# Optimization experiments

Measured on AMD Instinct MI355X. Metric: run time of the kernel, lower is better.

Reference implementation:

```python
import jax, jax.numpy as jnp
import numpy as np

BS, SL, N_AGENTS, OBS_DIM, STATE_DIM, N_EDGES, HID = 32, 512, 32, 96, 1024, 64, 256


def _hgcn(w_line, x, H):
    # x: [B, n, 1]; H: [B, n, E]. Faithful to torch HGCN:
    # A = D^{-1/2} H |W| B^{-1} H^T D^{-1/2}, with D, B built from detached H/|W|,
    # inf entries (from 0^{-1} / 0^{-0.5}) zeroed. Diagonal matmuls are implicit scalings.
    w_abs = jnp.abs(w_line)
    Hd = jax.lax.stop_gradient(H)
    d = jnp.einsum('bne,e->bn', Hd, jax.lax.stop_gradient(w_abs))  # [B, n]
    d_is = jnp.where(d > 0, jax.lax.rsqrt(jnp.where(d > 0, d, 1.0)), 0.0)
    b = jnp.sum(Hd, axis=-2)  # [B, E]
    b_inv = jnp.where(b > 0, 1.0 / jnp.where(b > 0, b, 1.0), 0.0)
    t = d_is[..., None] * x                       # D^{-1/2} x
    s = jnp.einsum('bne,bnk->bek', H, t)          # H^T (...)
    s = s * (w_abs[None, :] * b_inv)[..., None]   # |W| B^{-1} (diagonals commute)
    y = jnp.einsum('bne,bek->bnk', H, s)          # H (...)
    return d_is[..., None] * y                    # D^{-1/2} (...)


def _mlp(x, w1, b1, w2, b2):
    return jax.nn.relu(x @ w1 + b1) @ w2 + b2


def setup_inputs() -> dict:
    key = jax.random.key(0)
    ks = jax.random.split(key, 24)
    f = jax.random.normal
    inp = {
        'agent_qs': f(ks[0], (BS, SL, N_AGENTS), jnp.float32),
        'states': f(ks[1], (BS, SL, STATE_DIM), jnp.float32),
        'indiv_us': f(ks[2], (BS, SL, N_AGENTS, OBS_DIM), jnp.float32),
        'edge_W': f(ks[3], (OBS_DIM, N_EDGES), jnp.float32) * 0.1,
        'edge_b': f(ks[4], (N_EDGES,), jnp.float32) * 0.1,
        'wline1': 1.0 + 0.1 * f(ks[5], (N_EDGES,), jnp.float32),
        'wline2': 1.0 + 0.1 * f(ks[6], (N_EDGES,), jnp.float32),
    }
    names = ['hw1', 'hc1', 'hw', 'hc']
    outs = [N_AGENTS, N_AGENTS, N_AGENTS, 1]
    for i, (nm, od) in enumerate(zip(names, outs)):
        inp[nm + '_w1'] = f(ks[7 + 4 * i], (STATE_DIM, HID), jnp.float32) * 0.05
        inp[nm + '_b1'] = f(ks[8 + 4 * i], (HID,), jnp.float32) * 0.05
        inp[nm + '_w2'] = f(ks[9 + 4 * i], (HID, od), jnp.float32) * 0.05
        inp[nm + '_b2'] = f(ks[10 + 4 * i], (od,), jnp.float32) * 0.05
    return inp


def reference(agent_qs, states, indiv_us, edge_W, edge_b, wline1, wline2,
              hw1_w1, hw1_b1, hw1_w2, hw1_b2, hc1_w1, hc1_b1, hc1_w2, hc1_b2,
              hw_w1, hw_b1, hw_w2, hw_b2, hc_w1, hc_b1, hc_w2, hc_b2):
    bs, sl, n = agent_qs.shape
    q = agent_qs.reshape(-1, n)                               # [B, n]
    u = indiv_us.reshape(-1, n, indiv_us.shape[-1])           # [B, n, obs]
    s = states.reshape(-1, states.shape[-1])                  # [B, state_dim]
    H = jax.nn.relu(u @ edge_W + edge_b)                      # hyper_edge_net -> [B, n, E]
    x = q[..., None]                                          # node_features [B, n, 1]
    qs_tot = _hgcn(wline2, _hgcn(wline1, x, H), H)[..., 0]    # two stacked HGCN encoders
    w1 = jnp.abs(_mlp(s, hw1_w1, hw1_b1, hw1_w2, hw1_b2))
    c1 = _mlp(s, hc1_w1, hc1_b1, hc1_w2, hc1_b2)
    qt = jax.nn.elu(qs_tot * w1 + c1)
    w = jnp.abs(_mlp(s, hw_w1, hw_b1, hw_w2, hw_b2))
    c = _mlp(s, hc_w1, hc_b1, hc_w2, hc_b2)[..., 0]
    q_tot = jnp.sum(qt * w, axis=-1) + c
    return q_tot.reshape(bs, sl, 1)
```

## Files before the change

kernel.cpp:

```cpp
#include <hip/hip_runtime.h>
#include <cstdint>

typedef _Float16 f16;
typedef _Float16 f16x2 __attribute__((ext_vector_type(2)));
typedef _Float16 f16x4 __attribute__((ext_vector_type(4)));
typedef _Float16 f16x8 __attribute__((ext_vector_type(8)));
typedef float f32x4 __attribute__((ext_vector_type(4)));

#define AS1U const __attribute__((address_space(1))) unsigned int
#define AS3U __attribute__((address_space(3))) unsigned int

__device__ __forceinline__ void gload_lds16(const void* g, void* l) {
    __builtin_amdgcn_global_load_lds((AS1U*)g, (AS3U*)l, 16, 0, 0);
}

#define WSYNC() asm volatile("s_waitcnt lgkmcnt(0)" ::: "memory")

#define BATCH 16384
#define NAG   32
#define OBS   96
#define SDIM  1024
#define NE    64
#define HIDN  256
#define NH    1024

#define NB_ST 1024
#define NB_PW 256
#define NB_SM 101
#define NB_FRONT (NB_ST + NB_PW + NB_SM)

__global__ __launch_bounds__(256) void k_front(
    const float* __restrict__ states,
    const float* __restrict__ w1a, const float* __restrict__ w1b,
    const float* __restrict__ w1c, const float* __restrict__ w1d,
    const float* __restrict__ b1a, const float* __restrict__ b1b,
    const float* __restrict__ b1c, const float* __restrict__ b1d,
    const float* __restrict__ w2a, const float* __restrict__ w2b,
    const float* __restrict__ w2c, const float* __restrict__ w2d,
    f16* __restrict__ states16, f16* __restrict__ W1t, float* __restrict__ b1cat,
    f16* __restrict__ W2t, f16* __restrict__ hcw2) {
    __shared__ float tile[64 * 65];
    const int tid = threadIdx.x;
    int bid = blockIdx.x;

    if (bid < NB_ST) {
        int i = bid * 256 + tid;
        const int n4 = BATCH * SDIM / 4;
        const int stride = NB_ST * 256;
        for (; i < n4; i += stride) {
            float4 v = ((const float4*)states)[i];
            f16x4 h = { (f16)v.x, (f16)v.y, (f16)v.z, (f16)v.w };
            ((f16x4*)states16)[i] = h;
        }
        return;
    }
    bid -= NB_ST;
    if (bid < NB_PW) {
        int mlp = bid >> 6, rem = bid & 63, kt = rem >> 2, ct = rem & 3;
        const float* src = (mlp == 0) ? w1a : (mlp == 1) ? w1b : (mlp == 2) ? w1c : w1d;
        int k0 = kt * 64, c0 = ct * 64;
        for (int i = tid; i < 4096; i += 256) {
            int kk = i >> 6, cc = i & 63;
            tile[kk * 65 + cc] = src[(size_t)(k0 + kk) * 256 + c0 + cc];
        }
        __syncthreads();
        for (int i = tid; i < 4096; i += 256) {
            int cc = i >> 6, kk = i & 63;
            W1t[(size_t)(mlp * 256 + c0 + cc) * 1024 + k0 + kk] = (f16)tile[kk * 65 + cc];
        }
        return;
    }
    bid -= NB_PW;
    {
        int i = bid * 256 + tid;
        if (i < 24576) {
            int mp = i >> 13, rem = i & 8191, oo = rem >> 8, kk = rem & 255;
            const float* src = (mp == 0) ? w2a : (mp == 1) ? w2b : w2c;
            W2t[i] = (f16)src[kk * 32 + oo];
        } else if (i < 24832) {
            int k = i - 24576;
            hcw2[k] = (f16)w2d[k];
        } else if (i < 25856) {
            int n = i - 24832;
            int mlp = n >> 8, c = n & 255;
            const float* bsrc = (mlp == 0) ? b1a : (mlp == 1) ? b1b : (mlp == 2) ? b1c : b1d;
            b1cat[n] = bsrc[c];
        }
    }
}

__global__ __launch_bounds__(256) void k_gemm1(
    const f16* __restrict__ A, const f16* __restrict__ B,
    const float* __restrict__ b1cat, const f16* __restrict__ W2t,
    const f16* __restrict__ hcw2, float* __restrict__ Pp) {
    __shared__ __align__(16) char smem[33792];
    f16* As = (f16*)smem;
    f16* Bs = (f16*)(smem + 16384);
    f16* Ts = (f16*)smem;

    const int tid = threadIdx.x;
    const int w = tid >> 6, l = tid & 63;
    const int p = blockIdx.x;
    const int xcd = p & 7, slot = p >> 3;
    const int region = slot >> 6, rs = slot & 63;
    const int mt = (xcd * 2 + region) * 8 + (rs >> 3);
    const int nt = rs & 7;
    const int m0 = mt * 128, n0 = nt * 128;
    const int wm = w >> 1, wn = w & 1;
    const int lm = l & 15, lk = l >> 4;
    const int srow = l >> 3;
    const int scol = (l & 7) * 8;

    f32x4 acc[4][4];
    #pragma unroll
    for (int i = 0; i < 4; i++)
        #pragma unroll
        for (int j = 0; j < 4; j++) acc[i][j] = (f32x4){0.f, 0.f, 0.f, 0.f};

    for (int kt = 0; kt < 16; kt++) {
        #pragma unroll
        for (int i = 0; i < 4; i++) {
            int c = w * 4 + i;
            int row = c * 8 + srow;
            gload_lds16(&A[(size_t)(m0 + row) * 1024 + kt * 64 + scol], &As[c * 512]);
            gload_lds16(&B[(size_t)(n0 + row) * 1024 + kt * 64 + scol], &Bs[c * 512]);
        }
        __syncthreads();
        #pragma unroll
        for (int ks = 0; ks < 2; ks++) {
            f16x8 a[4], bb[4];
            #pragma unroll
            for (int i = 0; i < 4; i++)
                a[i] = *(const f16x8*)&As[(wm * 64 + i * 16 + lm) * 64 + ks * 32 + lk * 8];
            #pragma unroll
            for (int j = 0; j < 4; j++)
                bb[j] = *(const f16x8*)&Bs[(wn * 64 + j * 16 + lm) * 64 + ks * 32 + lk * 8];
            #pragma unroll
            for (int i = 0; i < 4; i++)
                #pragma unroll
                for (int j = 0; j < 4; j++)
                    acc[i][j] = __builtin_amdgcn_mfma_f32_16x16x32_f16(a[i], bb[j], acc[i][j], 0, 0, 0);
        }
        __syncthreads();
    }

    float bj[4];
    #pragma unroll
    for (int j = 0; j < 4; j++) bj[j] = b1cat[n0 + wn * 64 + j * 16 + lm];
    #pragma unroll
    for (int i = 0; i < 4; i++)
        #pragma unroll
        for (int r = 0; r < 4; r++) {
            int row = wm * 64 + i * 16 + lk * 4 + r;
            #pragma unroll
            for (int j = 0; j < 4; j++) {
                int col = wn * 64 + j * 16 + lm;
                float v = acc[i][j][r] + bj[j];
                Ts[row * 132 + col] = (f16)(v > 0.f ? v : 0.f);
            }
        }
    __syncthreads();

    const int mlp = nt >> 1, kh = nt & 1;
    const int rbase = w * 32;
    if (mlp < 3) {
        const f16* wb = W2t + mlp * 8192 + kh * 128;
        f32x4 acc2[2][2];
        acc2[0][0] = (f32x4){0,0,0,0}; acc2[0][1] = (f32x4){0,0,0,0};
        acc2[1][0] = (f32x4){0,0,0,0}; acc2[1][1] = (f32x4){0,0,0,0};
        #pragma unroll
        for (int ks = 0; ks < 4; ks++) {
            f16x8 b0 = *(const f16x8*)&wb[lm * 256 + ks * 32 + lk * 8];
            f16x8 b1 = *(const f16x8*)&wb[(16 + lm) * 256 + ks * 32 + lk * 8];
            #pragma unroll
            for (int i2 = 0; i2 < 2; i2++) {
                f16x8 a = *(const f16x8*)&Ts[(rbase + i2 * 16 + lm) * 132 + ks * 32 + lk * 8];
                acc2[i2][0] = __builtin_amdgcn_mfma_f32_16x16x32_f16(a, b0, acc2[i2][0], 0, 0, 0);
                acc2[i2][1] = __builtin_amdgcn_mfma_f32_16x16x32_f16(a, b1, acc2[i2][1], 0, 0, 0);
            }
        }
        #pragma unroll
        for (int i2 = 0; i2 < 2; i2++)
            #pragma unroll
            for (int j2 = 0; j2 < 2; j2++)
                #pragma unroll
                for (int r = 0; r < 4; r++)
                    Pp[((size_t)kh * BATCH + m0 + rbase + i2 * 16 + lk * 4 + r) * 104
                       + mlp * 32 + j2 * 16 + lm] = acc2[i2][j2][r];
    } else {
        const f16* hc = hcw2 + kh * 128;
        f32x4 acc2[2];
        acc2[0] = (f32x4){0,0,0,0}; acc2[1] = (f32x4){0,0,0,0};
        #pragma unroll
        for (int ks = 0; ks < 4; ks++) {
            f16x8 bz = (f16x8){0,0,0,0,0,0,0,0};
            if (lm == 0) bz = *(const f16x8*)&hc[ks * 32 + lk * 8];
            #pragma unroll
            for (int i2 = 0; i2 < 2; i2++) {
                f16x8 a = *(const f16x8*)&Ts[(rbase + i2 * 16 + lm) * 132 + ks * 32 + lk * 8];
                acc2[i2] = __builtin_amdgcn_mfma_f32_16x16x32_f16(a, bz, acc2[i2], 0, 0, 0);
            }
        }
        if (lm == 0)
            #pragma unroll
            for (int i2 = 0; i2 < 2; i2++)
                #pragma unroll
                for (int r = 0; r < 4; r++)
                    Pp[((size_t)kh * BATCH + m0 + rbase + i2 * 16 + lk * 4 + r) * 104 + 96]
                        = acc2[i2][r];
    }
}

__global__ __launch_bounds__(256, 5) void k_hgcn_ep(
    const float* __restrict__ agent_qs, const float* __restrict__ indiv_us,
    const float* __restrict__ edge_W, const float* __restrict__ edge_b,
    const float* __restrict__ wline1, const float* __restrict__ wline2,
    const float* __restrict__ Pp,
    const float* __restrict__ hw1_b2, const float* __restrict__ hc1_b2,
    const float* __restrict__ hw_b2, const float* __restrict__ hc_b2,
    float* __restrict__ out) {
    __shared__ __align__(16) char arena[32512];
    f16*   eWs   = (f16*)arena;
    float* swa   = (float*)(arena + 13312);
    f16*   HsB   = (f16*)(arena + 13824);
    f16*   svB   = (f16*)(arena + 30720);
    f16*   sttB  = (f16*)(arena + 31232);
    f16*   sdisB = (f16*)(arena + 31488);
    f16*   sbinvB= (f16*)(arena + 32000);

    const int tid = threadIdx.x;
    const int w = tid >> 6, l = tid & 63;
    const int b = blockIdx.x * 4 + w;
    f16* Hw    = HsB + w * (32 * 66);
    f16* sv    = svB + w * 64;
    f16* stt   = sttB + w * 32;
    f16* sdis  = sdisB + w * 64;
    f16* sbinv = sbinvB + w * 64;

    const int nn = l & 31, half = l >> 5;

    float pa0 = 0.f, pa1 = 0.f, pc0 = 0.f, pc1 = 0.f, pw0 = 0.f, pw1 = 0.f;
    float p96a = 0.f, p96b = 0.f, bw1 = 0.f, bc1 = 0.f, bww = 0.f, bhc = 0.f;
    if (half == 0) {
        const float* p0 = Pp + (size_t)b * 104;
        const float* p1 = Pp + (size_t)(BATCH + b) * 104;
        pa0 = p0[nn];      pa1 = p1[nn];
        pc0 = p0[32 + nn]; pc1 = p1[32 + nn];
        pw0 = p0[64 + nn]; pw1 = p1[64 + nn];
        p96a = p0[96];     p96b = p1[96];
        bw1 = hw1_b2[nn];  bc1 = hc1_b2[nn];
        bww = hw_b2[nn];   bhc = hc_b2[0];
    }
    float q = agent_qs[(size_t)b * 32 + nn];

    for (int i = tid; i < 6144; i += 256) {
        int k = i >> 6, n = i & 63;
        eWs[n * 104 + k] = (f16)edge_W[i];
    }
    if (tid < 64) swa[tid] = fabsf(wline1[tid]);
    else if (tid < 128) swa[tid] = fabsf(wline2[tid - 64]);
    __syncthreads();

    const int lm = l & 15, lk = l >> 4;
    const float* ub = indiv_us + (size_t)b * (NAG * OBS);

    #pragma unroll
    for (int mt = 0; mt < 2; mt++) {
        f16x8 af[3];
        #pragma unroll
        for (int ks = 0; ks < 3; ks++) {
            const float* up = ub + (mt * 16 + lm) * 96 + ks * 32 + lk * 8;
            float4 v0 = *(const float4*)up;
            float4 v1 = *(const float4*)(up + 4);
            af[ks] = (f16x8){ (f16)v0.x, (f16)v0.y, (f16)v0.z, (f16)v0.w,
                              (f16)v1.x, (f16)v1.y, (f16)v1.z, (f16)v1.w };
        }
        #pragma unroll
        for (int nt = 0; nt < 4; nt++) {
            f32x4 acc = {0.f, 0.f, 0.f, 0.f};
            #pragma unroll
            for (int ks = 0; ks < 3; ks++) {
                f16x8 bb = *(const f16x8*)&eWs[(nt * 16 + lm) * 104 + ks * 32 + lk * 8];
                acc = __builtin_amdgcn_mfma_f32_16x16x32_f16(af[ks], bb, acc, 0, 0, 0);
            }
            int col = nt * 16 + lm;
            float bias = edge_b[col];
            #pragma unroll
            for (int r = 0; r < 4; r++) {
                int row = mt * 16 + lk * 4 + r;
                float hv = acc[r] + bias;
                Hw[row * 66 + col] = (f16)(hv > 0.f ? hv : 0.f);
            }
        }
    }
    WSYNC();

    float bsum = 0.f;
    #pragma unroll
    for (int n = 0; n < 32; n++) bsum += (float)Hw[n * 66 + l];
    sbinv[l] = (f16)(bsum > 0.f ? 1.f / bsum : 0.f);

    float dd = 0.f;
    #pragma unroll 8
    for (int e2 = 0; e2 < 32; e2++) {
        f16x2 h2 = *(const f16x2*)&Hw[nn * 66 + e2 * 2];
        dd += (float)h2.x * swa[half * 64 + e2 * 2] + (float)h2.y * swa[half * 64 + e2 * 2 + 1];
    }
    float dis = dd > 0.f ? rsqrtf(dd) : 0.f;
    sdis[l] = (f16)dis;
    if (half == 0) stt[nn] = (f16)(dis * q);
    WSYNC();

    float s1 = 0.f;
    #pragma unroll
    for (int n = 0; n < 32; n++) s1 += (float)Hw[n * 66 + l] * (float)stt[n];
    sv[l] = (f16)(s1 * swa[l] * (float)sbinv[l]);
    WSYNC();

    float y1 = 0.f;
    #pragma unroll 8
    for (int e2 = 0; e2 < 32; e2++) {
        f16x2 h2 = *(const f16x2*)&Hw[nn * 66 + e2 * 2];
        f16x2 s2v = *(const f16x2*)&sv[e2 * 2];
        y1 += (float)h2.x * (float)s2v.x + (float)h2.y * (float)s2v.y;
    }
    float x2 = (float)sdis[nn] * y1;
    if (half == 0) stt[nn] = (f16)((float)sdis[32 + nn] * x2);
    WSYNC();

    float s2 = 0.f;
    #pragma unroll
    for (int n = 0; n < 32; n++) s2 += (float)Hw[n * 66 + l] * (float)stt[n];
    sv[l] = (f16)(s2 * swa[64 + l] * (float)sbinv[l]);
    WSYNC();

    float y2 = 0.f;
    #pragma unroll 8
    for (int e2 = 0; e2 < 32; e2++) {
        f16x2 h2 = *(const f16x2*)&Hw[nn * 66 + e2 * 2];
        f16x2 s2v = *(const f16x2*)&sv[e2 * 2];
        y2 += (float)h2.x * (float)s2v.x + (float)h2.y * (float)s2v.y;
    }

    float qsv = (float)sdis[32 + nn] * y2;
    float w1v = fabsf(pa0 + pa1 + bw1);
    float c1v = pc0 + pc1 + bc1;
    float wwv = fabsf(pw0 + pw1 + bww);
    float z = qsv * w1v + c1v;
    float qt = z > 0.f ? z : expm1f(z);
    float val = (half == 0) ? qt * wwv : 0.f;
    val += __shfl_xor(val, 1, 32);
    val += __shfl_xor(val, 2, 32);
    val += __shfl_xor(val, 4, 32);
    val += __shfl_xor(val, 8, 32);
    val += __shfl_xor(val, 16, 32);
    if (l == 0) out[b] = val + p96a + p96b + bhc;
}

extern "C" void kernel_launch(void* const* d_in, const int* in_sizes, int n_in,
                              void* d_out, int out_size, void* d_ws, size_t ws_size,
                              hipStream_t stream) {
    const float* agent_qs = (const float*)d_in[0];
    const float* states   = (const float*)d_in[1];
    const float* indiv_us = (const float*)d_in[2];
    const float* edge_W   = (const float*)d_in[3];
    const float* edge_b   = (const float*)d_in[4];
    const float* wline1   = (const float*)d_in[5];
    const float* wline2   = (const float*)d_in[6];
    const float* hw1_w1 = (const float*)d_in[7];
    const float* hw1_b1 = (const float*)d_in[8];
    const float* hw1_w2 = (const float*)d_in[9];
    const float* hw1_b2 = (const float*)d_in[10];
    const float* hc1_w1 = (const float*)d_in[11];
    const float* hc1_b1 = (const float*)d_in[12];
    const float* hc1_w2 = (const float*)d_in[13];
    const float* hc1_b2 = (const float*)d_in[14];
    const float* hw_w1  = (const float*)d_in[15];
    const float* hw_b1  = (const float*)d_in[16];
    const float* hw_w2  = (const float*)d_in[17];
    const float* hw_b2  = (const float*)d_in[18];
    const float* hc_w1  = (const float*)d_in[19];
    const float* hc_b1  = (const float*)d_in[20];
    const float* hc_w2  = (const float*)d_in[21];
    const float* hc_b2  = (const float*)d_in[22];

    char* ws = (char*)d_ws;
    size_t o_states16 = 0;
    size_t o_W1t  = o_states16 + (size_t)BATCH * SDIM * 2;
    size_t o_b1   = o_W1t + (size_t)NH * SDIM * 2;
    size_t o_W2t  = o_b1 + 4096;
    size_t o_hcw2 = o_W2t + 49152;
    size_t o_Pp   = o_hcw2 + 512;

    f16*   states16 = (f16*)(ws + o_states16);
    f16*   W1t      = (f16*)(ws + o_W1t);
    float* b1cat    = (float*)(ws + o_b1);
    f16*   W2t      = (f16*)(ws + o_W2t);
    f16*   hcw2     = (f16*)(ws + o_hcw2);
    float* Pp       = (float*)(ws + o_Pp);

    k_front<<<NB_FRONT, 256, 0, stream>>>(
        states,
        hw1_w1, hc1_w1, hw_w1, hc_w1, hw1_b1, hc1_b1, hw_b1, hc_b1,
        hw1_w2, hc1_w2, hw_w2, hc_w2,
        states16, W1t, b1cat, W2t, hcw2);
    k_gemm1<<<1024, 256, 0, stream>>>(states16, W1t, b1cat, W2t, hcw2, Pp);
    k_hgcn_ep<<<BATCH / 4, 256, 0, stream>>>(
        agent_qs, indiv_us, edge_W, edge_b, wline1, wline2, Pp,
        hw1_b2, hc1_b2, hw_b2, hc_b2, (float*)d_out);
}
```

Before: 136.5 us.

## Pre-pack GEMM operands in MFMA fragment order and load directly to registers

The front kernel now writes states and W1 in an MFMA-fragment-packed layout, so the GEMM kernel can load operand fragments straight from global memory into registers. This drops the LDS staging and the barriers in the k-loop. The trade-off is that the GEMM k-loop relies on cache and in-flight loads with no LDS reuse, so each wave re-reads shared fragments from L2. The HGCN epilogue also switches its intermediate scratch from fp16 to fp32 and drops the occupancy hint in launch_bounds.

```diff
diff --git a/kernel.cpp b/kernel.cpp
--- a/kernel.cpp
+++ b/kernel.cpp
@@ -6,13 +6,6 @@
 typedef _Float16 f16x4 __attribute__((ext_vector_type(4)));
 typedef _Float16 f16x8 __attribute__((ext_vector_type(8)));
 typedef float f32x4 __attribute__((ext_vector_type(4)));
-
-#define AS1U const __attribute__((address_space(1))) unsigned int
-#define AS3U __attribute__((address_space(3))) unsigned int
-
-__device__ __forceinline__ void gload_lds16(const void* g, void* l) {
-    __builtin_amdgcn_global_load_lds((AS1U*)g, (AS3U*)l, 16, 0, 0);
-}
 
 #define WSYNC() asm volatile("s_waitcnt lgkmcnt(0)" ::: "memory")
 
@@ -24,10 +17,10 @@
 #define HIDN  256
 #define NH    1024
 
-#define NB_ST 1024
-#define NB_PW 256
-#define NB_SM 101
-#define NB_FRONT (NB_ST + NB_PW + NB_SM)
+#define NB_CONV 512
+#define NB_PW   256
+#define NB_SM   101
+#define NB_FRONT (NB_CONV + NB_PW + NB_SM)
 
 __global__ __launch_bounds__(256) void k_front(
     const float* __restrict__ states,
@@ -37,36 +30,60 @@
     const float* __restrict__ b1c, const float* __restrict__ b1d,
     const float* __restrict__ w2a, const float* __restrict__ w2b,
     const float* __restrict__ w2c, const float* __restrict__ w2d,
-    f16* __restrict__ states16, f16* __restrict__ W1t, float* __restrict__ b1cat,
+    f16* __restrict__ App, f16* __restrict__ Bpp, float* __restrict__ b1cat,
     f16* __restrict__ W2t, f16* __restrict__ hcw2) {
-    __shared__ float tile[64 * 65];
+    __shared__ __align__(16) char arena[34816];
     const int tid = threadIdx.x;
+    const int w = tid >> 6, l = tid & 63;
     int bid = blockIdx.x;
 
-    if (bid < NB_ST) {
-        int i = bid * 256 + tid;
-        const int n4 = BATCH * SDIM / 4;
-        const int stride = NB_ST * 256;
-        for (; i < n4; i += stride) {
-            float4 v = ((const float4*)states)[i];
-            f16x4 h = { (f16)v.x, (f16)v.y, (f16)v.z, (f16)v.w };
-            ((f16x4*)states16)[i] = h;
+    if (bid < NB_CONV) {
+        float* tile = (float*)arena;
+        const int mt = bid >> 2, ktg = bid & 3;
+        const int row = tid >> 1, cb = (tid & 1) * 32;
+        for (int kq = 0; kq < 4; kq++) {
+            const int kt = ktg * 4 + kq;
+            const float* src = states + (size_t)(mt * 128 + row) * 1024 + kt * 64 + cb;
+            #pragma unroll
+            for (int q = 0; q < 8; q++)
+                *(float4*)&tile[row * 68 + cb + q * 4] = *(const float4*)(src + q * 4);
+            __syncthreads();
+            f16* dst = App + (size_t)(mt * 16 + kt) * 8192;
+            #pragma unroll
+            for (int cc = 0; cc < 4; cc++) {
+                const int c = w * 4 + cc;
+                const int i8 = c >> 1, ks = c & 1;
+                const float* tr = &tile[(i8 * 16 + (l & 15)) * 68 + ks * 32 + (l >> 4) * 8];
+                float4 u0 = *(const float4*)tr;
+                float4 u1 = *(const float4*)(tr + 4);
+                f16x8 h = { (f16)u0.x, (f16)u0.y, (f16)u0.z, (f16)u0.w,
+                            (f16)u1.x, (f16)u1.y, (f16)u1.z, (f16)u1.w };
+                *(f16x8*)(dst + c * 512 + l * 8) = h;
+            }
+            __syncthreads();
         }
         return;
     }
-    bid -= NB_ST;
+    bid -= NB_CONV;
     if (bid < NB_PW) {
-        int mlp = bid >> 6, rem = bid & 63, kt = rem >> 2, ct = rem & 3;
+        float* tile = (float*)arena;
+        const int mlp = bid >> 6, k64 = (bid >> 2) & 15, c64 = bid & 3;
         const float* src = (mlp == 0) ? w1a : (mlp == 1) ? w1b : (mlp == 2) ? w1c : w1d;
-        int k0 = kt * 64, c0 = ct * 64;
         for (int i = tid; i < 4096; i += 256) {
             int kk = i >> 6, cc = i & 63;
-            tile[kk * 65 + cc] = src[(size_t)(k0 + kk) * 256 + c0 + cc];
+            tile[kk * 65 + cc] = src[(size_t)(k64 * 64 + kk) * 256 + c64 * 64 + cc];
         }
         __syncthreads();
-        for (int i = tid; i < 4096; i += 256) {
-            int cc = i >> 6, kk = i & 63;
-            W1t[(size_t)(mlp * 256 + c0 + cc) * 1024 + k0 + kk] = (f16)tile[kk * 65 + cc];
+        const int nt = mlp * 2 + (c64 >> 1);
+        const int j8 = (c64 & 1) * 4 + w;
+        const int col = w * 16 + (l & 15);
+        #pragma unroll
+        for (int ks = 0; ks < 2; ks++) {
+            const int kk0 = ks * 32 + (l >> 4) * 8;
+            f16x8 h;
+            #pragma unroll
+            for (int e = 0; e < 8; e++) h[e] = (f16)tile[(kk0 + e) * 65 + col];
+            *(f16x8*)(Bpp + ((size_t)((nt * 16 + k64) * 8 + j8) * 2 + ks) * 512 + l * 8) = h;
         }
         return;
     }
@@ -89,27 +106,21 @@
     }
 }
 
-__global__ __launch_bounds__(256) void k_gemm1(
-    const f16* __restrict__ A, const f16* __restrict__ B,
+__global__ __launch_bounds__(256) void k_gemm(
+    const f16* __restrict__ App, const f16* __restrict__ Bpp,
     const float* __restrict__ b1cat, const f16* __restrict__ W2t,
     const f16* __restrict__ hcw2, float* __restrict__ Pp) {
-    __shared__ __align__(16) char smem[33792];
-    f16* As = (f16*)smem;
-    f16* Bs = (f16*)(smem + 16384);
-    f16* Ts = (f16*)smem;
+    __shared__ __align__(16) f16 Ts[128 * 132];
 
     const int tid = threadIdx.x;
     const int w = tid >> 6, l = tid & 63;
+    const int lm = l & 15, lk = l >> 4;
     const int p = blockIdx.x;
     const int xcd = p & 7, slot = p >> 3;
-    const int region = slot >> 6, rs = slot & 63;
-    const int mt = (xcd * 2 + region) * 8 + (rs >> 3);
-    const int nt = rs & 7;
+    const int mt = xcd * 16 + (slot >> 3);
+    const int nt = slot & 7;
     const int m0 = mt * 128, n0 = nt * 128;
     const int wm = w >> 1, wn = w & 1;
-    const int lm = l & 15, lk = l >> 4;
-    const int srow = l >> 3;
-    const int scol = (l & 7) * 8;
 
     f32x4 acc[4][4];
     #pragma unroll
@@ -117,31 +128,28 @@
         #pragma unroll
         for (int j = 0; j < 4; j++) acc[i][j] = (f32x4){0.f, 0.f, 0.f, 0.f};
 
+    const f16* Ab = App + ((size_t)mt * 16 * 16 + wm * 8) * 512 + l * 8;
+    const f16* Bb = Bpp + ((size_t)nt * 16 * 16 + wn * 8) * 512 + l * 8;
+
+    #pragma unroll 4
     for (int kt = 0; kt < 16; kt++) {
-        #pragma unroll
-        for (int i = 0; i < 4; i++) {
-            int c = w * 4 + i;
-            int row = c * 8 + srow;
-            gload_lds16(&A[(size_t)(m0 + row) * 1024 + kt * 64 + scol], &As[c * 512]);
-            gload_lds16(&B[(size_t)(n0 + row) * 1024 + kt * 64 + scol], &Bs[c * 512]);
-        }
-        __syncthreads();
-        #pragma unroll
-        for (int ks = 0; ks < 2; ks++) {
-            f16x8 a[4], bb[4];
-            #pragma unroll
-            for (int i = 0; i < 4; i++)
-                a[i] = *(const f16x8*)&As[(wm * 64 + i * 16 + lm) * 64 + ks * 32 + lk * 8];
-            #pragma unroll
-            for (int j = 0; j < 4; j++)
-                bb[j] = *(const f16x8*)&Bs[(wn * 64 + j * 16 + lm) * 64 + ks * 32 + lk * 8];
+        const f16* Ak = Ab + (size_t)kt * 8192;
+        const f16* Bk = Bb + (size_t)kt * 8192;
+        f16x8 af[4][2], bf[4][2];
+        #pragma unroll
+        for (int i = 0; i < 4; i++)
+            #pragma unroll
+            for (int ks = 0; ks < 2; ks++) {
+                af[i][ks] = *(const f16x8*)(Ak + (i * 2 + ks) * 512);
+                bf[i][ks] = *(const f16x8*)(Bk + (i * 2 + ks) * 512);
+            }
+        #pragma unroll
+        for (int ks = 0; ks < 2; ks++)
             #pragma unroll
             for (int i = 0; i < 4; i++)
                 #pragma unroll
                 for (int j = 0; j < 4; j++)
-                    acc[i][j] = __builtin_amdgcn_mfma_f32_16x16x32_f16(a[i], bb[j], acc[i][j], 0, 0, 0);
-        }
-        __syncthreads();
+                    acc[i][j] = __builtin_amdgcn_mfma_f32_16x16x32_f16(af[i][ks], bf[j][ks], acc[i][j], 0, 0, 0);
     }
 
     float bj[4];
@@ -211,7 +219,7 @@
     }
 }
 
-__global__ __launch_bounds__(256, 5) void k_hgcn_ep(
+__global__ __launch_bounds__(256) void k_hgcn_ep(
     const float* __restrict__ agent_qs, const float* __restrict__ indiv_us,
     const float* __restrict__ edge_W, const float* __restrict__ edge_b,
     const float* __restrict__ wline1, const float* __restrict__ wline2,
@@ -219,23 +227,23 @@
     const float* __restrict__ hw1_b2, const float* __restrict__ hc1_b2,
     const float* __restrict__ hw_b2, const float* __restrict__ hc_b2,
     float* __restrict__ out) {
-    __shared__ __align__(16) char arena[32512];
+    __shared__ __align__(16) char arena[34304];
     f16*   eWs   = (f16*)arena;
     float* swa   = (float*)(arena + 13312);
     f16*   HsB   = (f16*)(arena + 13824);
-    f16*   svB   = (f16*)(arena + 30720);
-    f16*   sttB  = (f16*)(arena + 31232);
-    f16*   sdisB = (f16*)(arena + 31488);
-    f16*   sbinvB= (f16*)(arena + 32000);
+    float* svB   = (float*)(arena + 30720);
+    float* sttB  = (float*)(arena + 31744);
+    float* sdisB = (float*)(arena + 32256);
+    float* sbinvB= (float*)(arena + 33280);
 
     const int tid = threadIdx.x;
     const int w = tid >> 6, l = tid & 63;
     const int b = blockIdx.x * 4 + w;
-    f16* Hw    = HsB + w * (32 * 66);
-    f16* sv    = svB + w * 64;
-    f16* stt   = sttB + w * 32;
-    f16* sdis  = sdisB + w * 64;
-    f16* sbinv = sbinvB + w * 64;
+    f16*   Hw    = HsB + w * (32 * 66);
+    float* sv    = svB + w * 64;
+    float* stt   = sttB + w * 32;
+    float* sdis  = sdisB + w * 64;
+    float* sbinv = sbinvB + w * 64;
 
     const int nn = l & 31, half = l >> 5;
 
@@ -298,7 +306,7 @@
     float bsum = 0.f;
     #pragma unroll
     for (int n = 0; n < 32; n++) bsum += (float)Hw[n * 66 + l];
-    sbinv[l] = (f16)(bsum > 0.f ? 1.f / bsum : 0.f);
+    sbinv[l] = bsum > 0.f ? 1.f / bsum : 0.f;
 
     float dd = 0.f;
     #pragma unroll 8
@@ -307,42 +315,40 @@
         dd += (float)h2.x * swa[half * 64 + e2 * 2] + (float)h2.y * swa[half * 64 + e2 * 2 + 1];
     }
     float dis = dd > 0.f ? rsqrtf(dd) : 0.f;
-    sdis[l] = (f16)dis;
-    if (half == 0) stt[nn] = (f16)(dis * q);
+    sdis[l] = dis;
+    if (half == 0) stt[nn] = dis * q;
     WSYNC();
 
     float s1 = 0.f;
     #pragma unroll
-    for (int n = 0; n < 32; n++) s1 += (float)Hw[n * 66 + l] * (float)stt[n];
-    sv[l] = (f16)(s1 * swa[l] * (float)sbinv[l]);
+    for (int n = 0; n < 32; n++) s1 += (float)Hw[n * 66 + l] * stt[n];
+    sv[l] = s1 * swa[l] * sbinv[l];
     WSYNC();
 
     float y1 = 0.f;
     #pragma unroll 8
     for (int e2 = 0; e2 < 32; e2++) {
         f16x2 h2 = *(const f16x2*)&Hw[nn * 66 + e2 * 2];
-        f16x2 s2v = *(const f16x2*)&sv[e2 * 2];
-        y1 += (float)h2.x * (float)s2v.x + (float)h2.y * (float)s2v.y;
-    }
-    float x2 = (float)sdis[nn] * y1;
-    if (half == 0) stt[nn] = (f16)((float)sdis[32 + nn] * x2);
+        y1 += (float)h2.x * sv[e2 * 2] + (float)h2.y * sv[e2 * 2 + 1];
+    }
+    float x2 = sdis[nn] * y1;
+    if (half == 0) stt[nn] = sdis[32 + nn] * x2;
     WSYNC();
 
     float s2 = 0.f;
     #pragma unroll
-    for (int n = 0; n < 32; n++) s2 += (float)Hw[n * 66 + l] * (float)stt[n];
-    sv[l] = (f16)(s2 * swa[64 + l] * (float)sbinv[l]);
+    for (int n = 0; n < 32; n++) s2 += (float)Hw[n * 66 + l] * stt[n];
+    sv[l] = s2 * swa[64 + l] * sbinv[l];
     WSYNC();
 
     float y2 = 0.f;
     #pragma unroll 8
     for (int e2 = 0; e2 < 32; e2++) {
         f16x2 h2 = *(const f16x2*)&Hw[nn * 66 + e2 * 2];
-        f16x2 s2v = *(const f16x2*)&sv[e2 * 2];
-        y2 += (float)h2.x * (float)s2v.x + (float)h2.y * (float)s2v.y;
-    }
-
-    float qsv = (float)sdis[32 + nn] * y2;
+        y2 += (float)h2.x * sv[e2 * 2] + (float)h2.y * sv[e2 * 2 + 1];
+    }
+
+    float qsv = sdis[32 + nn] * y2;
     float w1v = fabsf(pa0 + pa1 + bw1);
     float c1v = pc0 + pc1 + bc1;
     float wwv = fabsf(pw0 + pw1 + bww);
@@ -385,26 +391,26 @@
     const float* hc_b2  = (const float*)d_in[22];
 
     char* ws = (char*)d_ws;
-    size_t o_states16 = 0;
-    size_t o_W1t  = o_states16 + (size_t)BATCH * SDIM * 2;
-    size_t o_b1   = o_W1t + (size_t)NH * SDIM * 2;
+    size_t o_App  = 0;
+    size_t o_Bpp  = o_App + (size_t)BATCH * SDIM * 2;
+    size_t o_b1   = o_Bpp + (size_t)NH * SDIM * 2;
     size_t o_W2t  = o_b1 + 4096;
     size_t o_hcw2 = o_W2t + 49152;
     size_t o_Pp   = o_hcw2 + 512;
 
-    f16*   states16 = (f16*)(ws + o_states16);
-    f16*   W1t      = (f16*)(ws + o_W1t);
-    float* b1cat    = (float*)(ws + o_b1);
-    f16*   W2t      = (f16*)(ws + o_W2t);
-    f16*   hcw2     = (f16*)(ws + o_hcw2);
-    float* Pp       = (float*)(ws + o_Pp);
+    f16*   App    = (f16*)(ws + o_App);
+    f16*   Bpp    = (f16*)(ws + o_Bpp);
+    float* b1cat  = (float*)(ws + o_b1);
+    f16*   W2t    = (f16*)(ws + o_W2t);
+    f16*   hcw2   = (f16*)(ws + o_hcw2);
+    float* Pp     = (float*)(ws + o_Pp);
 
     k_front<<<NB_FRONT, 256, 0, stream>>>(
         states,
         hw1_w1, hc1_w1, hw_w1, hc_w1, hw1_b1, hc1_b1, hw_b1, hc_b1,
         hw1_w2, hc1_w2, hw_w2, hc_w2,
-        states16, W1t, b1cat, W2t, hcw2);
-    k_gemm1<<<1024, 256, 0, stream>>>(states16, W1t, b1cat, W2t, hcw2, Pp);
+        App, Bpp, b1cat, W2t, hcw2);
+    k_gemm<<<1024, 256, 0, stream>>>(App, Bpp, b1cat, W2t, hcw2, Pp);
     k_hgcn_ep<<<BATCH / 4, 256, 0, stream>>>(
         agent_qs, indiv_us, edge_W, edge_b, wline1, wline2, Pp,
         hw1_b2, hc1_b2, hw_b2, hc_b2, (float*)d_out);
```

Result: slower. 155.0 us (+13.5%).

## Use 256x256 double-buffered GEMM tiles so each block owns a full MLP hidden

Applied to the files above, without the earlier changes.

The first-layer GEMM now uses 512-thread blocks with 256x256 tiles and double-buffered LDS loads, so the next K slice is prefetched while the current one is computed. Each block covers one MLP's full 256-wide hidden layer, so the second-layer projection writes a single partial instead of two K-halves, and the epilogue kernel reads half as many partials. The HGCN intermediates in LDS are switched from f16 to f32, and the occupancy hint on that kernel is dropped. The cost is 128KB of shared memory per block, which allows only one block per CU, and just 256 blocks in the grid.

```diff
diff --git a/kernel.cpp b/kernel.cpp
--- a/kernel.cpp
+++ b/kernel.cpp
@@ -89,129 +89,132 @@
     }
 }
 
-__global__ __launch_bounds__(256) void k_gemm1(
+__global__ __launch_bounds__(512) void k_gemm(
     const f16* __restrict__ A, const f16* __restrict__ B,
     const float* __restrict__ b1cat, const f16* __restrict__ W2t,
     const f16* __restrict__ hcw2, float* __restrict__ Pp) {
-    __shared__ __align__(16) char smem[33792];
-    f16* As = (f16*)smem;
-    f16* Bs = (f16*)(smem + 16384);
-    f16* Ts = (f16*)smem;
+    __shared__ __align__(16) char smem[131072];
+    f16* Asb = (f16*)smem;
+    f16* Bsb = (f16*)(smem + 65536);
+    f16* Ts  = (f16*)smem;
 
     const int tid = threadIdx.x;
     const int w = tid >> 6, l = tid & 63;
+    const int lm = l & 15, lk = l >> 4;
+    const int wm = w >> 2, wn = w & 3;
     const int p = blockIdx.x;
-    const int xcd = p & 7, slot = p >> 3;
-    const int region = slot >> 6, rs = slot & 63;
-    const int mt = (xcd * 2 + region) * 8 + (rs >> 3);
-    const int nt = rs & 7;
-    const int m0 = mt * 128, n0 = nt * 128;
-    const int wm = w >> 1, wn = w & 1;
-    const int lm = l & 15, lk = l >> 4;
-    const int srow = l >> 3;
-    const int scol = (l & 7) * 8;
-
-    f32x4 acc[4][4];
-    #pragma unroll
-    for (int i = 0; i < 4; i++)
+    const int xcd = p & 7, s = p >> 3;
+    const int mt = xcd * 8 + (s >> 2);
+    const int nt = s & 3;
+    const int m0 = mt * 256, n0 = nt * 256;
+    const int c0 = w * 4;
+    const int srow = l >> 3, scol = (l & 7) * 8;
+
+    f32x4 acc[8][4];
+    #pragma unroll
+    for (int i = 0; i < 8; i++)
         #pragma unroll
         for (int j = 0; j < 4; j++) acc[i][j] = (f32x4){0.f, 0.f, 0.f, 0.f};
 
+    #pragma unroll
+    for (int i = 0; i < 4; i++) {
+        int cc = c0 + i;
+        gload_lds16(&A[(size_t)(m0 + cc * 8 + srow) * 1024 + scol], &Asb[cc * 512]);
+        gload_lds16(&B[(size_t)(n0 + cc * 8 + srow) * 1024 + scol], &Bsb[cc * 512]);
+    }
+    __syncthreads();
+
+    int cur = 0;
     for (int kt = 0; kt < 16; kt++) {
-        #pragma unroll
-        for (int i = 0; i < 4; i++) {
-            int c = w * 4 + i;
-            int row = c * 8 + srow;
-            gload_lds16(&A[(size_t)(m0 + row) * 1024 + kt * 64 + scol], &As[c * 512]);
-            gload_lds16(&B[(size_t)(n0 + row) * 1024 + kt * 64 + scol], &Bs[c * 512]);
-        }
-        __syncthreads();
+        if (kt < 15) {
+            f16* Ad = Asb + (cur ^ 1) * 16384;
+            f16* Bd = Bsb + (cur ^ 1) * 16384;
+            #pragma unroll
+            for (int i = 0; i < 4; i++) {
+                int cc = c0 + i;
+                gload_lds16(&A[(size_t)(m0 + cc * 8 + srow) * 1024 + (kt + 1) * 64 + scol], &Ad[cc * 512]);
+                gload_lds16(&B[(size_t)(n0 + cc * 8 + srow) * 1024 + (kt + 1) * 64 + scol], &Bd[cc * 512]);
+            }
+        }
+        const f16* As_ = Asb + cur * 16384;
+        const f16* Bs_ = Bsb + cur * 16384;
         #pragma unroll
         for (int ks = 0; ks < 2; ks++) {
-            f16x8 a[4], bb[4];
-            #pragma unroll
-            for (int i = 0; i < 4; i++)
-                a[i] = *(const f16x8*)&As[(wm * 64 + i * 16 + lm) * 64 + ks * 32 + lk * 8];
+            f16x8 af[8], bf[4];
+            #pragma unroll
+            for (int i = 0; i < 8; i++)
+                af[i] = *(const f16x8*)&As_[(wm * 128 + i * 16 + lm) * 64 + ks * 32 + lk * 8];
             #pragma unroll
             for (int j = 0; j < 4; j++)
-                bb[j] = *(const f16x8*)&Bs[(wn * 64 + j * 16 + lm) * 64 + ks * 32 + lk * 8];
-            #pragma unroll
-            for (int i = 0; i < 4; i++)
+                bf[j] = *(const f16x8*)&Bs_[(wn * 64 + j * 16 + lm) * 64 + ks * 32 + lk * 8];
+            #pragma unroll
+            for (int i = 0; i < 8; i++)
                 #pragma unroll
                 for (int j = 0; j < 4; j++)
-                    acc[i][j] = __builtin_amdgcn_mfma_f32_16x16x32_f16(a[i], bb[j], acc[i][j], 0, 0, 0);
+                    acc[i][j] = __builtin_amdgcn_mfma_f32_16x16x32_f16(af[i], bf[j], acc[i][j], 0, 0, 0);
         }
         __syncthreads();
+        cur ^= 1;
     }
 
     float bj[4];
     #pragma unroll
     for (int j = 0; j < 4; j++) bj[j] = b1cat[n0 + wn * 64 + j * 16 + lm];
-    #pragma unroll
-    for (int i = 0; i < 4; i++)
-        #pragma unroll
-        for (int r = 0; r < 4; r++) {
-            int row = wm * 64 + i * 16 + lk * 4 + r;
-            #pragma unroll
-            for (int j = 0; j < 4; j++) {
-                int col = wn * 64 + j * 16 + lm;
-                float v = acc[i][j][r] + bj[j];
-                Ts[row * 132 + col] = (f16)(v > 0.f ? v : 0.f);
+    const int mlp = nt;
+
+    #pragma unroll
+    for (int pass = 0; pass < 2; pass++) {
+        if (wm == pass) {
+            #pragma unroll
+            for (int i = 0; i < 8; i++)
+                #pragma unroll
+                for (int r = 0; r < 4; r++) {
+                    int rl = i * 16 + lk * 4 + r;
+                    #pragma unroll
+                    for (int j = 0; j < 4; j++) {
+                        float v = acc[i][j][r] + bj[j];
+                        Ts[rl * 264 + wn * 64 + j * 16 + lm] = (f16)(v > 0.f ? v : 0.f);
+                    }
+                }
+        }
+        __syncthreads();
+        const int grow = m0 + pass * 128 + w * 16;
+        if (mlp < 3) {
+            const f16* wb = W2t + mlp * 8192;
+            f32x4 acc2[2];
+            acc2[0] = (f32x4){0, 0, 0, 0}; acc2[1] = (f32x4){0, 0, 0, 0};
+            #pragma unroll
+            for (int ks = 0; ks < 8; ks++) {
+                f16x8 a  = *(const f16x8*)&Ts[(w * 16 + lm) * 264 + ks * 32 + lk * 8];
+                f16x8 b0 = *(const f16x8*)&wb[lm * 256 + ks * 32 + lk * 8];
+                f16x8 b1 = *(const f16x8*)&wb[(16 + lm) * 256 + ks * 32 + lk * 8];
+                acc2[0] = __builtin_amdgcn_mfma_f32_16x16x32_f16(a, b0, acc2[0], 0, 0, 0);
+                acc2[1] = __builtin_amdgcn_mfma_f32_16x16x32_f16(a, b1, acc2[1], 0, 0, 0);
             }
-        }
-    __syncthreads();
-
-    const int mlp = nt >> 1, kh = nt & 1;
-    const int rbase = w * 32;
-    if (mlp < 3) {
-        const f16* wb = W2t + mlp * 8192 + kh * 128;
-        f32x4 acc2[2][2];
-        acc2[0][0] = (f32x4){0,0,0,0}; acc2[0][1] = (f32x4){0,0,0,0};
-        acc2[1][0] = (f32x4){0,0,0,0}; acc2[1][1] = (f32x4){0,0,0,0};
-        #pragma unroll
-        for (int ks = 0; ks < 4; ks++) {
-            f16x8 b0 = *(const f16x8*)&wb[lm * 256 + ks * 32 + lk * 8];
-            f16x8 b1 = *(const f16x8*)&wb[(16 + lm) * 256 + ks * 32 + lk * 8];
-            #pragma unroll
-            for (int i2 = 0; i2 < 2; i2++) {
-                f16x8 a = *(const f16x8*)&Ts[(rbase + i2 * 16 + lm) * 132 + ks * 32 + lk * 8];
-                acc2[i2][0] = __builtin_amdgcn_mfma_f32_16x16x32_f16(a, b0, acc2[i2][0], 0, 0, 0);
-                acc2[i2][1] = __builtin_amdgcn_mfma_f32_16x16x32_f16(a, b1, acc2[i2][1], 0, 0, 0);
-            }
-        }
-        #pragma unroll
-        for (int i2 = 0; i2 < 2; i2++)
             #pragma unroll
             for (int j2 = 0; j2 < 2; j2++)
                 #pragma unroll
                 for (int r = 0; r < 4; r++)
-                    Pp[((size_t)kh * BATCH + m0 + rbase + i2 * 16 + lk * 4 + r) * 104
-                       + mlp * 32 + j2 * 16 + lm] = acc2[i2][j2][r];
-    } else {
-        const f16* hc = hcw2 + kh * 128;
-        f32x4 acc2[2];
-        acc2[0] = (f32x4){0,0,0,0}; acc2[1] = (f32x4){0,0,0,0};
-        #pragma unroll
-        for (int ks = 0; ks < 4; ks++) {
-            f16x8 bz = (f16x8){0,0,0,0,0,0,0,0};
-            if (lm == 0) bz = *(const f16x8*)&hc[ks * 32 + lk * 8];
-            #pragma unroll
-            for (int i2 = 0; i2 < 2; i2++) {
-                f16x8 a = *(const f16x8*)&Ts[(rbase + i2 * 16 + lm) * 132 + ks * 32 + lk * 8];
-                acc2[i2] = __builtin_amdgcn_mfma_f32_16x16x32_f16(a, bz, acc2[i2], 0, 0, 0);
+                    Pp[(size_t)(grow + lk * 4 + r) * 104 + mlp * 32 + j2 * 16 + lm] = acc2[j2][r];
+        } else {
+            f32x4 acc2 = (f32x4){0, 0, 0, 0};
+            #pragma unroll
+            for (int ks = 0; ks < 8; ks++) {
+                f16x8 a = *(const f16x8*)&Ts[(w * 16 + lm) * 264 + ks * 32 + lk * 8];
+                f16x8 bz = (f16x8){0, 0, 0, 0, 0, 0, 0, 0};
+                if (lm == 0) bz = *(const f16x8*)&hcw2[ks * 32 + lk * 8];
+                acc2 = __builtin_amdgcn_mfma_f32_16x16x32_f16(a, bz, acc2, 0, 0, 0);
             }
-        }
-        if (lm == 0)
-            #pragma unroll
-            for (int i2 = 0; i2 < 2; i2++)
+            if (lm == 0)
                 #pragma unroll
                 for (int r = 0; r < 4; r++)
-                    Pp[((size_t)kh * BATCH + m0 + rbase + i2 * 16 + lk * 4 + r) * 104 + 96]
-                        = acc2[i2][r];
+                    Pp[(size_t)(grow + lk * 4 + r) * 104 + 96] = acc2[r];
+        }
+        if (pass == 0) __syncthreads();
     }
 }
 
-__global__ __launch_bounds__(256, 5) void k_hgcn_ep(
+__global__ __launch_bounds__(256) void k_hgcn_ep(
     const float* __restrict__ agent_qs, const float* __restrict__ indiv_us,
     const float* __restrict__ edge_W, const float* __restrict__ edge_b,
     const float* __restrict__ wline1, const float* __restrict__ wline2,
@@ -219,35 +222,34 @@
     const float* __restrict__ hw1_b2, const float* __restrict__ hc1_b2,
     const float* __restrict__ hw_b2, const float* __restrict__ hc_b2,
     float* __restrict__ out) {
-    __shared__ __align__(16) char arena[32512];
+    __shared__ __align__(16) char arena[34304];
     f16*   eWs   = (f16*)arena;
     float* swa   = (float*)(arena + 13312);
     f16*   HsB   = (f16*)(arena + 13824);
-    f16*   svB   = (f16*)(arena + 30720);
-    f16*   sttB  = (f16*)(arena + 31232);
-    f16*   sdisB = (f16*)(arena + 31488);
-    f16*   sbinvB= (f16*)(arena + 32000);
+    float* svB   = (float*)(arena + 30720);
+    float* sttB  = (float*)(arena + 31744);
+    float* sdisB = (float*)(arena + 32256);
+    float* sbinvB= (float*)(arena + 33280);
 
     const int tid = threadIdx.x;
     const int w = tid >> 6, l = tid & 63;
     const int b = blockIdx.x * 4 + w;
-    f16* Hw    = HsB + w * (32 * 66);
-    f16* sv    = svB + w * 64;
-    f16* stt   = sttB + w * 32;
-    f16* sdis  = sdisB + w * 64;
-    f16* sbinv = sbinvB + w * 64;
+    f16*   Hw    = HsB + w * (32 * 66);
+    float* sv    = svB + w * 64;
+    float* stt   = sttB + w * 32;
+    float* sdis  = sdisB + w * 64;
+    float* sbinv = sbinvB + w * 64;
 
     const int nn = l & 31, half = l >> 5;
 
-    float pa0 = 0.f, pa1 = 0.f, pc0 = 0.f, pc1 = 0.f, pw0 = 0.f, pw1 = 0.f;
-    float p96a = 0.f, p96b = 0.f, bw1 = 0.f, bc1 = 0.f, bww = 0.f, bhc = 0.f;
+    float pa0 = 0.f, pc0 = 0.f, pw0 = 0.f;
+    float p96a = 0.f, bw1 = 0.f, bc1 = 0.f, bww = 0.f, bhc = 0.f;
     if (half == 0) {
         const float* p0 = Pp + (size_t)b * 104;
-        const float* p1 = Pp + (size_t)(BATCH + b) * 104;
-        pa0 = p0[nn];      pa1 = p1[nn];
-        pc0 = p0[32 + nn]; pc1 = p1[32 + nn];
-        pw0 = p0[64 + nn]; pw1 = p1[64 + nn];
-        p96a = p0[96];     p96b = p1[96];
+        pa0 = p0[nn];
+        pc0 = p0[32 + nn];
+        pw0 = p0[64 + nn];
+        p96a = p0[96];
         bw1 = hw1_b2[nn];  bc1 = hc1_b2[nn];
         bww = hw_b2[nn];   bhc = hc_b2[0];
     }
@@ -298,7 +300,7 @@
     float bsum = 0.f;
     #pragma unroll
     for (int n = 0; n < 32; n++) bsum += (float)Hw[n * 66 + l];
-    sbinv[l] = (f16)(bsum > 0.f ? 1.f / bsum : 0.f);
+    sbinv[l] = bsum > 0.f ? 1.f / bsum : 0.f;
 
     float dd = 0.f;
     #pragma unroll 8
@@ -307,45 +309,43 @@
         dd += (float)h2.x * swa[half * 64 + e2 * 2] + (float)h2.y * swa[half * 64 + e2 * 2 + 1];
     }
     float dis = dd > 0.f ? rsqrtf(dd) : 0.f;
-    sdis[l] = (f16)dis;
-    if (half == 0) stt[nn] = (f16)(dis * q);
+    sdis[l] = dis;
+    if (half == 0) stt[nn] = dis * q;
     WSYNC();
 
     float s1 = 0.f;
     #pragma unroll
-    for (int n = 0; n < 32; n++) s1 += (float)Hw[n * 66 + l] * (float)stt[n];
-    sv[l] = (f16)(s1 * swa[l] * (float)sbinv[l]);
+    for (int n = 0; n < 32; n++) s1 += (float)Hw[n * 66 + l] * stt[n];
+    sv[l] = s1 * swa[l] * sbinv[l];
     WSYNC();
 
     float y1 = 0.f;
     #pragma unroll 8
     for (int e2 = 0; e2 < 32; e2++) {
         f16x2 h2 = *(const f16x2*)&Hw[nn * 66 + e2 * 2];
-        f16x2 s2v = *(const f16x2*)&sv[e2 * 2];
-        y1 += (float)h2.x * (float)s2v.x + (float)h2.y * (float)s2v.y;
-    }
-    float x2 = (float)sdis[nn] * y1;
-    if (half == 0) stt[nn] = (f16)((float)sdis[32 + nn] * x2);
+        y1 += (float)h2.x * sv[e2 * 2] + (float)h2.y * sv[e2 * 2 + 1];
+    }
+    float x2 = sdis[nn] * y1;
+    if (half == 0) stt[nn] = sdis[32 + nn] * x2;
     WSYNC();
 
     float s2 = 0.f;
     #pragma unroll
-    for (int n = 0; n < 32; n++) s2 += (float)Hw[n * 66 + l] * (float)stt[n];
-    sv[l] = (f16)(s2 * swa[64 + l] * (float)sbinv[l]);
+    for (int n = 0; n < 32; n++) s2 += (float)Hw[n * 66 + l] * stt[n];
+    sv[l] = s2 * swa[64 + l] * sbinv[l];
     WSYNC();
 
     float y2 = 0.f;
     #pragma unroll 8
     for (int e2 = 0; e2 < 32; e2++) {
         f16x2 h2 = *(const f16x2*)&Hw[nn * 66 + e2 * 2];
-        f16x2 s2v = *(const f16x2*)&sv[e2 * 2];
-        y2 += (float)h2.x * (float)s2v.x + (float)h2.y * (float)s2v.y;
-    }
-
-    float qsv = (float)sdis[32 + nn] * y2;
-    float w1v = fabsf(pa0 + pa1 + bw1);
-    float c1v = pc0 + pc1 + bc1;
-    float wwv = fabsf(pw0 + pw1 + bww);
+        y2 += (float)h2.x * sv[e2 * 2] + (float)h2.y * sv[e2 * 2 + 1];
+    }
+
+    float qsv = sdis[32 + nn] * y2;
+    float w1v = fabsf(pa0 + bw1);
+    float c1v = pc0 + bc1;
+    float wwv = fabsf(pw0 + bww);
     float z = qsv * w1v + c1v;
     float qt = z > 0.f ? z : expm1f(z);
     float val = (half == 0) ? qt * wwv : 0.f;
@@ -354,7 +354,7 @@
     val += __shfl_xor(val, 4, 32);
     val += __shfl_xor(val, 8, 32);
     val += __shfl_xor(val, 16, 32);
-    if (l == 0) out[b] = val + p96a + p96b + bhc;
+    if (l == 0) out[b] = val + p96a + bhc;
 }
 
 extern "C" void kernel_launch(void* const* d_in, const int* in_sizes, int n_in,
@@ -404,7 +404,7 @@
         hw1_w1, hc1_w1, hw_w1, hc_w1, hw1_b1, hc1_b1, hw_b1, hc_b1,
         hw1_w2, hc1_w2, hw_w2, hc_w2,
         states16, W1t, b1cat, W2t, hcw2);
-    k_gemm1<<<1024, 256, 0, stream>>>(states16, W1t, b1cat, W2t, hcw2, Pp);
+    k_gemm<<<256, 512, 0, stream>>>(states16, W1t, b1cat, W2t, hcw2, Pp);
     k_hgcn_ep<<<BATCH / 4, 256, 0, stream>>>(
         agent_qs, indiv_us, edge_W, edge_b, wline1, wline2, Pp,
         hw1_b2, hc1_b2, hw_b2, hc_b2, (float*)d_out);
```

New measurement: 124.1 us. 9.1% less time.
